# Kernel optimization log

Hardware: AMD Instinct MI355X
Metric: run time of the kernel (lower is better)

The kernel has to match this reference:

```python
import jax, jax.numpy as jnp
from jax import lax
import numpy as np

STYLE_STRENGTH = 1.0
PATCH = 3
TOL = 1e-14


def covsqrt_mean(feature, inverse=False):
    # feature: [b, c, h, w]; matches torch covsqrt_mean with eigenvalue truncation.
    b, c, h, w = feature.shape
    f = feature.reshape(b, c, h * w)
    mean = jnp.mean(f, axis=2, keepdims=True)
    zm = f - mean
    cov = jnp.einsum('bcn,bdn->bcd', zm, zm)  # unnormalized covariance, [b,c,c]
    evals, evecs = jnp.linalg.eigh(cov)       # ascending evals, like torch
    p = -0.5 if inverse else 0.5
    # torch keeps evals[k:] where k is the first index with eval > tol; since
    # evals are sorted ascending this equals masking evals > tol.
    mask = evals > TOL
    d = jnp.where(mask, jnp.where(mask, evals, 1.0) ** p, 0.0)
    covsqrt = jnp.einsum('bij,bj,bkj->bik', evecs, d, evecs)
    return covsqrt, mean


def whitening(feature):
    b, c, h, w = feature.shape
    inv_cs, mean = covsqrt_mean(feature, inverse=True)
    out = jnp.einsum('bcd,bdn->bcn', inv_cs, feature.reshape(b, c, -1) - mean)
    return out.reshape(b, c, h, w)


def coloring(feature, target):
    b, c, h, w = feature.shape
    cs, mean = covsqrt_mean(target, inverse=False)
    out = jnp.einsum('bcd,bdn->bcn', cs, feature.reshape(b, c, -1)) + mean
    return out.reshape(b, c, h, w)


def extract_kernels(feat, k):
    # feat [b,c,h,w] -> per-location style patches as conv kernels [b, h*w, c, k, k]
    b, c, h, w = feat.shape
    pad = (k - 1) // 2
    fp = jnp.pad(feat, ((0, 0), (0, 0), (pad, pad), (pad, pad)))
    # stack the k*k shifted views: [b, c, h, w, k*k] in (ky, kx) row-major order,
    # matching torch unfold(2,k).unfold(3,k) flattening.
    patches = jnp.stack([fp[:, :, dy:dy + h, dx:dx + w]
                         for dy in range(k) for dx in range(k)], axis=-1)
    return patches.reshape(b, c, h * w, k * k).transpose(0, 2, 1, 3).reshape(b, h * w, c, k, k)


def reassemble(norm_c, norm_s, k):
    b, c, h, w = norm_c.shape
    ker = extract_kernels(norm_s, k)                                  # [b, hw_s, c, k, k]
    knorm = jnp.sqrt(jnp.sum(ker ** 2, axis=(2, 3, 4), keepdims=True))
    pad = (k - 1) // 2

    def conv_one(feat, kk):
        # feat [c,h,w], kk [hw_s,c,k,k] -> score [hw_s,h,w]
        x = jnp.pad(feat, ((0, 0), (pad, pad), (pad, pad)))[None]
        return lax.conv_general_dilated(x, kk, (1, 1), 'VALID')[0]

    score = jax.vmap(conv_one)(norm_c, ker / knorm)                   # [b, hw_s, h, w]
    idx = jnp.argmax(score, axis=1)                                   # [b, h, w]
    onehot = jax.nn.one_hot(idx, score.shape[1], dtype=score.dtype).transpose(0, 3, 1, 2)

    def deconv_one(oh, kk):
        # conv_transpose2d(padded onehot, kk, padding=k-1) == VALID conv with
        # spatially flipped kernel (in/out channels swapped).
        x = jnp.pad(oh, ((0, 0), (pad, pad), (pad, pad)))[None]        # [1, hw_s, h+2p, w+2p]
        wf = jnp.flip(kk, axis=(2, 3)).transpose(1, 0, 2, 3)           # [c, hw_s, k, k]
        return lax.conv_general_dilated(x, wf, (1, 1), 'VALID')[0]     # [c, h, w]

    out = jax.vmap(deconv_one)(onehot, ker)                           # [b, c, h, w]
    # overlap-count normalization: separable box filter of ones
    cnt_h = jnp.convolve(jnp.ones(h, out.dtype), jnp.ones(k, out.dtype), mode='same')
    cnt_w = jnp.convolve(jnp.ones(w, out.dtype), jnp.ones(k, out.dtype), mode='same')
    deconv_norm = (cnt_h[:, None] * cnt_w[None, :])[None, None]
    return out / deconv_norm


def setup_inputs() -> dict:
    key = jax.random.key(0)
    k1, k2 = jax.random.split(key)
    b, ch, h, w = 2, 256, 48, 48
    c = jax.random.normal(k1, (b, ch, h, w), dtype=jnp.float32)
    s = jax.random.normal(k2, (b, ch, h, w), dtype=jnp.float32)
    return {'c': c, 's': s}


def reference(c, s):
    norm_c = whitening(c)
    norm_s = whitening(s)
    rF = reassemble(norm_c, norm_s, PATCH)
    sF = coloring(rF, s)
    return (1.0 - STYLE_STRENGTH) * c + STYLE_STRENGTH * sF
```

## Files before the change

### kernel.cpp

```cpp
#include <hip/hip_runtime.h>
#include <math.h>

#define HW 2304
#define NC 256
#define NPIX 2500
#define NPIXP 2560
#define MATSZ 65536
#define NS_ITERS 5
#define NSLAB 6
#define KSLAB 384
#define PMSZ (2560 * 256)
#define GSZ ((u64)NPIXP * NPIXP)

typedef unsigned long long u64;
typedef unsigned short ushortt;
typedef __attribute__((ext_vector_type(8))) short bhalf8;
typedef __attribute__((ext_vector_type(4))) float f32x4;

__global__ void mean_kernel(const float* __restrict__ c, const float* __restrict__ s,
                            double* __restrict__ mean, double* __restrict__ snorm) {
  int ch = blockIdx.x, m = blockIdx.y;
  const float* src = (m < 2 ? c + m * (NC * HW) : s + (m - 2) * (NC * HW)) + ch * HW;
  double acc = 0.0, acc2 = 0.0;
  for (int n = threadIdx.x; n < HW; n += 64) {
    double v = (double)src[n];
    acc += v; acc2 += v * v;
  }
  for (int o = 32; o > 0; o >>= 1) {
    acc += __shfl_down(acc, o);
    acc2 += __shfl_down(acc2, o);
  }
  if (threadIdx.x == 0) {
    mean[m * NC + ch] = acc / (double)HW;
    double diag = acc2 - acc * acc / (double)HW;
    atomicAdd(&snorm[m], 1.25 * diag / 256.0);
  }
}

__launch_bounds__(256)
__global__ void cov_part(const float* __restrict__ c, const float* __restrict__ s,
                         float* __restrict__ covp) {
  int z = blockIdx.z;
  int m = z / NSLAB, slab = z % NSLAB;
  const float* src = (m < 2 ? c + m * (NC * HW) : s + (m - 2) * (NC * HW));
  int i0 = blockIdx.y * 64, j0 = blockIdx.x * 64;
  int kb = slab * KSLAB;
  __shared__ float As[16][64], Bs[16][64];
  int tx = threadIdx.x, ty = threadIdx.y;
  int tid = ty * 16 + tx;
  int li = tid >> 2;
  int lk4 = tid & 3;
  float acc[4][4] = {};
  for (int kc = 0; kc < KSLAB; kc += 16) {
    __syncthreads();
    float4 va = *(const float4*)&src[(u64)(i0 + li) * HW + kb + kc + lk4 * 4];
    float4 vb = *(const float4*)&src[(u64)(j0 + li) * HW + kb + kc + lk4 * 4];
    As[lk4 * 4 + 0][li] = va.x; As[lk4 * 4 + 1][li] = va.y;
    As[lk4 * 4 + 2][li] = va.z; As[lk4 * 4 + 3][li] = va.w;
    Bs[lk4 * 4 + 0][li] = vb.x; Bs[lk4 * 4 + 1][li] = vb.y;
    Bs[lk4 * 4 + 2][li] = vb.z; Bs[lk4 * 4 + 3][li] = vb.w;
    __syncthreads();
    #pragma unroll
    for (int kk = 0; kk < 16; ++kk) {
      float4 a = *(const float4*)&As[kk][ty * 4];
      float4 b = *(const float4*)&Bs[kk][tx * 4];
      float av[4] = {a.x, a.y, a.z, a.w};
      float bv[4] = {b.x, b.y, b.z, b.w};
      #pragma unroll
      for (int i = 0; i < 4; ++i)
        #pragma unroll
        for (int j = 0; j < 4; ++j) acc[i][j] += av[i] * bv[j];
    }
  }
  float* Cp = covp + (u64)z * MATSZ;
  #pragma unroll
  for (int i = 0; i < 4; ++i) {
    float4 v = make_float4(acc[i][0], acc[i][1], acc[i][2], acc[i][3]);
    *(float4*)&Cp[(i0 + ty * 4 + i) * NC + j0 + tx * 4] = v;
  }
}

__global__ void cov_reduce(const float* __restrict__ covp, const double* __restrict__ mean,
                           const double* __restrict__ snorm,
                           float* __restrict__ Y0, float* __restrict__ Z1) {
  int m = blockIdx.y;
  int row = blockIdx.x, col = threadIdx.x;
  int e = row * 256 + col;
  float v = 0.0f;
  #pragma unroll
  for (int slab = 0; slab < NSLAB; ++slab)
    v += covp[(u64)(m * NSLAB + slab) * MATSZ + e];
  double mi = mean[m * NC + row], mj = mean[m * NC + col];
  float res = (float)((double)v - (double)HW * mi * mj);
  float inv = (float)(1.0 / snorm[m]);
  float y0 = res * inv;
  Y0[m * MATSZ + e] = y0;
  Z1[m * MATSZ + e] = ((row == col) ? 1.5f : 0.0f) - 0.5f * y0;
}

__launch_bounds__(256)
__global__ void ns_gemm_Y(const float* __restrict__ Y0, const float* __restrict__ T0,
                          float* __restrict__ Y1) {
  int m = blockIdx.z;
  const float* A = Y0 + m * MATSZ;
  const float* B = T0 + m * MATSZ;
  float* Cp = Y1 + m * MATSZ;
  int m0 = blockIdx.y * 32, n0 = blockIdx.x * 32;
  __shared__ float As[32][33], Bs[32][33];
  int tx = threadIdx.x, ty = threadIdx.y;
  int tid = ty * 16 + tx;
  float acc[2][2] = {};
  for (int k0 = 0; k0 < 256; k0 += 32) {
    __syncthreads();
    #pragma unroll
    for (int l = 0; l < 4; ++l) {
      int idx = tid + l * 256;
      int r = idx >> 5, cc = idx & 31;
      As[r][cc] = A[(m0 + r) * NC + k0 + cc];
      Bs[r][cc] = B[(k0 + r) * NC + n0 + cc];
    }
    __syncthreads();
    #pragma unroll
    for (int kk = 0; kk < 32; ++kk) {
      float a0 = As[ty][kk], a1 = As[ty + 16][kk];
      float b0 = Bs[kk][tx], b1 = Bs[kk][tx + 16];
      acc[0][0] += a0 * b0; acc[0][1] += a0 * b1;
      acc[1][0] += a1 * b0; acc[1][1] += a1 * b1;
    }
  }
  #pragma unroll
  for (int i = 0; i < 2; ++i)
    #pragma unroll
    for (int j = 0; j < 2; ++j)
      Cp[(m0 + ty + 16 * i) * NC + n0 + tx + 16 * j] = acc[i][j];
}

__launch_bounds__(256)
__global__ void ns_gemm_T(const float* __restrict__ Zc, const float* __restrict__ Yc,
                          float* __restrict__ T) {
  int m = blockIdx.z;
  const float* A = Zc + m * MATSZ;
  const float* B = Yc + m * MATSZ;
  int m0 = blockIdx.y * 32, n0 = blockIdx.x * 32;
  __shared__ float As[32][33], Bs[32][33];
  int tx = threadIdx.x, ty = threadIdx.y;
  int tid = ty * 16 + tx;
  float acc[2][2] = {};
  for (int k0 = 0; k0 < 256; k0 += 32) {
    __syncthreads();
    #pragma unroll
    for (int l = 0; l < 4; ++l) {
      int idx = tid + l * 256;
      int r = idx >> 5, cc = idx & 31;
      As[r][cc] = A[(m0 + r) * NC + k0 + cc];
      Bs[r][cc] = B[(k0 + r) * NC + n0 + cc];
    }
    __syncthreads();
    #pragma unroll
    for (int kk = 0; kk < 32; ++kk) {
      float a0 = As[ty][kk], a1 = As[ty + 16][kk];
      float b0 = Bs[kk][tx], b1 = Bs[kk][tx + 16];
      acc[0][0] += a0 * b0; acc[0][1] += a0 * b1;
      acc[1][0] += a1 * b0; acc[1][1] += a1 * b1;
    }
  }
  float* Cp = T + m * MATSZ;
  #pragma unroll
  for (int i = 0; i < 2; ++i)
    #pragma unroll
    for (int j = 0; j < 2; ++j) {
      int row = m0 + ty + 16 * i, col = n0 + tx + 16 * j;
      Cp[row * NC + col] = (row == col ? 1.5f : 0.0f) - 0.5f * acc[i][j];
    }
}

__launch_bounds__(256)
__global__ void ns_gemm_YZ(const float* __restrict__ Yc, const float* __restrict__ Zc,
                           const float* __restrict__ T,
                           float* __restrict__ Yn, float* __restrict__ Zn) {
  int z = blockIdx.z;
  int m = z & 3;
  bool isY = (z < 4);
  const float* A = isY ? (Yc + m * MATSZ) : (T + m * MATSZ);
  const float* B = isY ? (T + m * MATSZ) : (Zc + m * MATSZ);
  float* Cp = isY ? (Yn + m * MATSZ) : (Zn + m * MATSZ);
  int m0 = blockIdx.y * 32, n0 = blockIdx.x * 32;
  __shared__ float As[32][33], Bs[32][33];
  int tx = threadIdx.x, ty = threadIdx.y;
  int tid = ty * 16 + tx;
  float acc[2][2] = {};
  for (int k0 = 0; k0 < 256; k0 += 32) {
    __syncthreads();
    #pragma unroll
    for (int l = 0; l < 4; ++l) {
      int idx = tid + l * 256;
      int r = idx >> 5, cc = idx & 31;
      As[r][cc] = A[(m0 + r) * NC + k0 + cc];
      Bs[r][cc] = B[(k0 + r) * NC + n0 + cc];
    }
    __syncthreads();
    #pragma unroll
    for (int kk = 0; kk < 32; ++kk) {
      float a0 = As[ty][kk], a1 = As[ty + 16][kk];
      float b0 = Bs[kk][tx], b1 = Bs[kk][tx + 16];
      acc[0][0] += a0 * b0; acc[0][1] += a0 * b1;
      acc[1][0] += a1 * b0; acc[1][1] += a1 * b1;
    }
  }
  #pragma unroll
  for (int i = 0; i < 2; ++i)
    #pragma unroll
    for (int j = 0; j < 2; ++j)
      Cp[(m0 + ty + 16 * i) * NC + n0 + tx + 16 * j] = acc[i][j];
}

__launch_bounds__(256)
__global__ void whiten_kernel(const float* __restrict__ c, const float* __restrict__ s,
                              const float* __restrict__ Zf,
                              const double* __restrict__ snorm, const double* __restrict__ mean,
                              float* __restrict__ padC_cf, float* __restrict__ padS_cf,
                              float* __restrict__ padS_cl) {
  int mat = blockIdx.z;
  const float* src = (mat < 2 ? c + mat * (NC * HW) : s + (mat - 2) * (NC * HW));
  const float* A = Zf + mat * MATSZ;
  const double* mn = mean + mat * NC;
  float wscale = (float)(1.0 / sqrt(snorm[mat]));
  int m0 = blockIdx.y * 64, n0 = blockIdx.x * 64;
  __shared__ float As[16][68], Bs[16][68];
  int tid = threadIdx.x;
  int tx = tid & 15, ty = tid >> 4;
  int li = tid >> 2, lk4 = tid & 3;
  int kr = tid >> 4, p4 = (tid & 15) * 4;
  float acc[4][4] = {};
  for (int kc = 0; kc < 256; kc += 16) {
    __syncthreads();
    float4 va = *(const float4*)&A[(u64)(m0 + li) * NC + kc + lk4 * 4];
    As[lk4 * 4 + 0][li] = va.x; As[lk4 * 4 + 1][li] = va.y;
    As[lk4 * 4 + 2][li] = va.z; As[lk4 * 4 + 3][li] = va.w;
    float mk = (float)mn[kc + kr];
    float4 vb = *(const float4*)&src[(u64)(kc + kr) * HW + n0 + p4];
    vb.x -= mk; vb.y -= mk; vb.z -= mk; vb.w -= mk;
    *(float4*)&Bs[kr][p4] = vb;
    __syncthreads();
    #pragma unroll
    for (int kk = 0; kk < 16; ++kk) {
      float4 a = *(const float4*)&As[kk][ty * 4];
      float4 b = *(const float4*)&Bs[kk][tx * 4];
      float av[4] = {a.x, a.y, a.z, a.w};
      float bv[4] = {b.x, b.y, b.z, b.w};
      #pragma unroll
      for (int i = 0; i < 4; ++i)
        #pragma unroll
        for (int j = 0; j < 4; ++j) acc[i][j] += av[i] * bv[j];
    }
  }
  #pragma unroll
  for (int i = 0; i < 4; ++i) {
    int row = m0 + ty * 4 + i;
    #pragma unroll
    for (int j = 0; j < 4; ++j) {
      int n = n0 + tx * 4 + j;
      float v = acc[i][j] * wscale;
      int y = n / 48, x = n % 48;
      int ppos = (y + 1) * 50 + (x + 1);
      if (mat < 2) {
        padC_cf[(u64)mat * (NC * NPIXP) + row * NPIXP + ppos] = v;
      } else {
        padS_cf[(u64)(mat - 2) * (NC * NPIXP) + row * NPIXP + ppos] = v;
        padS_cl[(u64)(mat - 2) * (NPIX * NC) + ppos * NC + row] = v;
      }
    }
  }
}

__launch_bounds__(256)
__global__ void tsplit_kernel(const float* __restrict__ padC_cf, const float* __restrict__ padS_cf,
                              ushortt* __restrict__ padCk_hi, ushortt* __restrict__ padCk_lo,
                              ushortt* __restrict__ padSk_hi, ushortt* __restrict__ padSk_lo,
                              float* __restrict__ ssq) {
  int p0 = blockIdx.x * 64;
  int by = blockIdx.y;
  const float* src = (by < 2) ? padC_cf + (u64)by * (NC * NPIXP)
                              : padS_cf + (u64)(by - 2) * (NC * NPIXP);
  ushortt* dhi = (by < 2) ? padCk_hi + (u64)by * PMSZ : padSk_hi + (u64)(by - 2) * PMSZ;
  ushortt* dlo = (by < 2) ? padCk_lo + (u64)by * PMSZ : padSk_lo + (u64)(by - 2) * PMSZ;
  __shared__ float Tk[64][68];
  int tid = threadIdx.x;
  int rr = tid >> 4, c4 = (tid & 15) * 4;
  int p = tid >> 2, kg = (tid & 3) * 16;
  float sq = 0.0f;
  for (int ks = 0; ks < 256; ks += 64) {
    __syncthreads();
    #pragma unroll
    for (int it = 0; it < 4; ++it) {
      int r = rr + it * 16;
      *(float4*)&Tk[r][c4] = *(const float4*)&src[(u64)(ks + r) * NPIXP + p0 + c4];
    }
    __syncthreads();
    __align__(16) ushortt h[16], lo[16];
    #pragma unroll
    for (int e = 0; e < 16; ++e) {
      float v = Tk[kg + e][p];
      sq += v * v;
      unsigned bb = __float_as_uint(v);
      unsigned hu = (bb + 0x7FFFu + ((bb >> 16) & 1u)) >> 16;
      float hf = __uint_as_float(hu << 16);
      float rres = v - hf;
      unsigned lb = __float_as_uint(rres);
      unsigned lu = (lb + 0x7FFFu + ((lb >> 16) & 1u)) >> 16;
      h[e] = (ushortt)hu;
      lo[e] = (ushortt)lu;
    }
    u64 off = (u64)(p0 + p) * 256 + ks + kg;
    *(uint4*)&dhi[off] = *(const uint4*)&h[0];
    *(uint4*)&dhi[off + 8] = *(const uint4*)&h[8];
    *(uint4*)&dlo[off] = *(const uint4*)&lo[0];
    *(uint4*)&dlo[off + 8] = *(const uint4*)&lo[8];
  }
  sq += __shfl_down(sq, 2);
  sq += __shfl_down(sq, 1);
  if (by >= 2 && (tid & 3) == 0 && (p0 + p) < NPIX)
    ssq[(u64)(by - 2) * NPIX + p0 + p] = sq;
}

__launch_bounds__(256)
__global__ void gram_mfma(const ushortt* __restrict__ Ah_b, const ushortt* __restrict__ Al_b,
                          const ushortt* __restrict__ Bh_b, const ushortt* __restrict__ Bl_b,
                          float* __restrict__ Gb) {
  int bz = blockIdx.z;
  const ushortt* Ah_g = Ah_b + (u64)bz * PMSZ;
  const ushortt* Al_g = Al_b + (u64)bz * PMSZ;
  const ushortt* Bh_g = Bh_b + (u64)bz * PMSZ;
  const ushortt* Bl_g = Bl_b + (u64)bz * PMSZ;
  float* G = Gb + (u64)bz * GSZ;
  __shared__ ushortt As_hi[128 * 32], As_lo[128 * 32], Bs_hi[64 * 32], Bs_lo[64 * 32];
  int tid = threadIdx.x;
  int wv = tid >> 6, l = tid & 63, lr = l & 15, lk = l >> 4;
  int p0 = blockIdx.x * 128, q0 = blockIdx.y * 64;
  int arow = tid >> 2;
  int apart = (tid & 3) * 8;
  const ushortt* pAh0 = Ah_g + (u64)(p0 + arow) * 256 + apart;
  const ushortt* pAh1 = Ah_g + (u64)(p0 + arow + 64) * 256 + apart;
  const ushortt* pAl0 = Al_g + (u64)(p0 + arow) * 256 + apart;
  const ushortt* pAl1 = Al_g + (u64)(p0 + arow + 64) * 256 + apart;
  const ushortt* pBh  = Bh_g + (u64)(q0 + arow) * 256 + apart;
  const ushortt* pBl  = Bl_g + (u64)(q0 + arow) * 256 + apart;
  float4 rAh0 = *(const float4*)pAh0;
  float4 rAh1 = *(const float4*)pAh1;
  float4 rAl0 = *(const float4*)pAl0;
  float4 rAl1 = *(const float4*)pAl1;
  float4 rBh  = *(const float4*)pBh;
  float4 rBl  = *(const float4*)pBl;
  f32x4 acc[2][4];
  #pragma unroll
  for (int a = 0; a < 2; ++a)
    #pragma unroll
    for (int b = 0; b < 4; ++b)
      #pragma unroll
      for (int e = 0; e < 4; ++e) acc[a][b][e] = 0.0f;
  for (int k0 = 0; k0 < 256; k0 += 32) {
    __syncthreads();
    *(float4*)&As_hi[arow * 32 + apart] = rAh0;
    *(float4*)&As_hi[(arow + 64) * 32 + apart] = rAh1;
    *(float4*)&As_lo[arow * 32 + apart] = rAl0;
    *(float4*)&As_lo[(arow + 64) * 32 + apart] = rAl1;
    *(float4*)&Bs_hi[arow * 32 + apart] = rBh;
    *(float4*)&Bs_lo[arow * 32 + apart] = rBl;
    __syncthreads();
    if (k0 + 32 < 256) {
      rAh0 = *(const float4*)(pAh0 + k0 + 32);
      rAh1 = *(const float4*)(pAh1 + k0 + 32);
      rAl0 = *(const float4*)(pAl0 + k0 + 32);
      rAl1 = *(const float4*)(pAl1 + k0 + 32);
      rBh  = *(const float4*)(pBh + k0 + 32);
      rBl  = *(const float4*)(pBl + k0 + 32);
    }
    bhalf8 Ah[2], Al[2], Bh[4], Bl[4];
    #pragma unroll
    for (int a = 0; a < 2; ++a) {
      int off = (wv * 32 + a * 16 + lr) * 32 + lk * 8;
      Ah[a] = *(const bhalf8*)&As_hi[off];
      Al[a] = *(const bhalf8*)&As_lo[off];
    }
    #pragma unroll
    for (int b = 0; b < 4; ++b) {
      int off = (b * 16 + lr) * 32 + lk * 8;
      Bh[b] = *(const bhalf8*)&Bs_hi[off];
      Bl[b] = *(const bhalf8*)&Bs_lo[off];
    }
    #pragma unroll
    for (int a = 0; a < 2; ++a)
      #pragma unroll
      for (int b = 0; b < 4; ++b) {
        acc[a][b] = __builtin_amdgcn_mfma_f32_16x16x32_bf16(Ah[a], Bh[b], acc[a][b], 0, 0, 0);
        acc[a][b] = __builtin_amdgcn_mfma_f32_16x16x32_bf16(Ah[a], Bl[b], acc[a][b], 0, 0, 0);
        acc[a][b] = __builtin_amdgcn_mfma_f32_16x16x32_bf16(Al[a], Bh[b], acc[a][b], 0, 0, 0);
      }
  }
  #pragma unroll
  for (int a = 0; a < 2; ++a)
    #pragma unroll
    for (int b = 0; b < 4; ++b)
      #pragma unroll
      for (int r = 0; r < 4; ++r) {
        int p = p0 + wv * 32 + a * 16 + lk * 4 + r;
        int q = q0 + b * 16 + lr;
        G[(u64)p * NPIXP + q] = acc[a][b][r];
      }
}

__launch_bounds__(256)
__global__ void scoremax_kernel(const float* __restrict__ Gb, const float* __restrict__ ssq,
                                u64* __restrict__ rmax) {
  int y = blockIdx.x, ys = blockIdx.y, b = blockIdx.z;
  const float* G = Gb + (u64)b * GSZ;
  const float* sq = ssq + (u64)b * NPIX;
  __shared__ float Gt[3][50][50];
  __shared__ float sc[48][48];
  __shared__ float sr[152];
  __shared__ float rkl[48];
  int tid = threadIdx.x;
  for (int t = tid; t < 7500; t += 256) {
    int dy = t / 2500, rem = t % 2500;
    int u = rem / 50, v = rem - u * 50;
    Gt[dy][u][v] = G[(u64)((y + dy) * 50 + u) * NPIXP + (ys + dy) * 50 + v];
  }
  if (tid < 150) {
    int dy = tid / 50, v = tid - dy * 50;
    sr[dy * 50 + v] = sq[(ys + dy) * 50 + v];
  }
  __syncthreads();
  if (tid < 48) {
    float t = 0.0f;
    #pragma unroll
    for (int dy = 0; dy < 3; ++dy)
      #pragma unroll
      for (int dx = 0; dx < 3; ++dx) t += sr[dy * 50 + tid + dx];
    rkl[tid] = 1.0f / sqrtf(t);
  }
  __syncthreads();
  #pragma unroll
  for (int k = 0; k < 9; ++k) {
    int idx = tid + k * 256;
    int x = idx / 48, xs = idx - x * 48;
    float v = 0.0f;
    #pragma unroll
    for (int dy = 0; dy < 3; ++dy)
      #pragma unroll
      for (int dx = 0; dx < 3; ++dx)
        v += Gt[dy][x + dx][xs + dx];
    sc[x][xs] = v * rkl[xs];
  }
  __syncthreads();
  if (tid < 48) {
    float best = -1e30f; int bxs = 0;
    for (int xs = 0; xs < 48; ++xs) {
      float v = sc[tid][xs];
      if (v > best) { best = v; bxs = xs; }
    }
    int ps = ys * 48 + bxs;
    unsigned ub = __float_as_uint(best);
    unsigned enc = (ub & 0x80000000u) ? ~ub : (ub | 0x80000000u);
    u64 key = ((u64)enc << 32) | (u64)(2303 - ps);
    atomicMax(&rmax[(u64)b * HW + y * 48 + tid], key);
  }
}

__global__ void reassemble_kernel(const float* __restrict__ padS_cl, const u64* __restrict__ rmax,
                                  float* __restrict__ rF_cl) {
  int pix = blockIdx.x, b = blockIdx.y;
  int y = pix / 48, x = pix % 48;
  const u64* rm = rmax + (u64)b * HW;
  const float* S = padS_cl + (u64)b * (NPIX * NC);
  int ch = threadIdx.x;
  float sum = 0.0f;
  #pragma unroll
  for (int i = 0; i < 3; ++i)
    #pragma unroll
    for (int j = 0; j < 3; ++j) {
      int yn = y + 1 - i, xn = x + 1 - j;
      if (yn >= 0 && yn < 48 && xn >= 0 && xn < 48) {
        int ps = 2303 - (int)(unsigned)(rm[yn * 48 + xn] & 0xFFFFFFFFu);
        int ys = ps / 48, xs = ps % 48;
        sum += S[((ys + i) * 50 + xs + j) * NC + ch];
      }
    }
  float cy = (y == 0 || y == 47) ? 2.0f : 3.0f;
  float cx = (x == 0 || x == 47) ? 2.0f : 3.0f;
  rF_cl[(u64)b * (HW * NC) + pix * NC + ch] = sum / (cy * cx);
}

__launch_bounds__(256)
__global__ void coloring_kernel(const float* __restrict__ Yf, const double* __restrict__ snorm,
                                const double* __restrict__ mean, const float* __restrict__ rF_cl,
                                float* __restrict__ out) {
  int b = blockIdx.z;
  const float* A = Yf + (2 + b) * MATSZ;
  const float* Bp = rF_cl + (u64)b * (HW * NC);
  const double* mn = mean + (2 + b) * NC;
  float cscale = (float)sqrt(snorm[2 + b]);
  int m0 = blockIdx.y * 64, n0 = blockIdx.x * 64;
  __shared__ float As[16][68], Bs[16][68];
  int tid = threadIdx.x;
  int tx = tid & 15, ty = tid >> 4;
  int li = tid >> 2, lk4 = tid & 3;
  int pix = tid >> 2, kq = (tid & 3) * 4;
  float acc[4][4] = {};
  for (int kc = 0; kc < 256; kc += 16) {
    __syncthreads();
    float4 va = *(const float4*)&A[(u64)(m0 + li) * NC + kc + lk4 * 4];
    As[lk4 * 4 + 0][li] = va.x; As[lk4 * 4 + 1][li] = va.y;
    As[lk4 * 4 + 2][li] = va.z; As[lk4 * 4 + 3][li] = va.w;
    float4 vb = *(const float4*)&Bp[(u64)(n0 + pix) * NC + kc + kq];
    Bs[kq + 0][pix] = vb.x; Bs[kq + 1][pix] = vb.y;
    Bs[kq + 2][pix] = vb.z; Bs[kq + 3][pix] = vb.w;
    __syncthreads();
    #pragma unroll
    for (int kk = 0; kk < 16; ++kk) {
      float4 a = *(const float4*)&As[kk][ty * 4];
      float4 b2 = *(const float4*)&Bs[kk][tx * 4];
      float av[4] = {a.x, a.y, a.z, a.w};
      float bv[4] = {b2.x, b2.y, b2.z, b2.w};
      #pragma unroll
      for (int i = 0; i < 4; ++i)
        #pragma unroll
        for (int j = 0; j < 4; ++j) acc[i][j] += av[i] * bv[j];
    }
  }
  #pragma unroll
  for (int i = 0; i < 4; ++i) {
    int row = m0 + ty * 4 + i;
    float madd = (float)mn[row];
    float4 v = make_float4(acc[i][0] * cscale + madd, acc[i][1] * cscale + madd,
                           acc[i][2] * cscale + madd, acc[i][3] * cscale + madd);
    *(float4*)&out[(u64)b * (NC * HW) + (u64)row * HW + n0 + tx * 4] = v;
  }
}

extern "C" void kernel_launch(void* const* d_in, const int* in_sizes, int n_in,
                              void* d_out, int out_size, void* d_ws, size_t ws_size,
                              hipStream_t stream) {
  const float* c = (const float*)d_in[0];
  const float* s = (const float*)d_in[1];
  float* out = (float*)d_out;

  char* ws = (char*)d_ws;
  size_t off = 0;
  auto alloc = [&](size_t bytes) {
    void* p = ws + off;
    off = (off + bytes + 255) & ~(size_t)255;
    return p;
  };
  double* mean   = (double*)alloc(4 * NC * sizeof(double));
  float* covp    = (float*)alloc((size_t)4 * NSLAB * MATSZ * sizeof(float));
  float* Ya      = (float*)alloc((size_t)4 * MATSZ * sizeof(float));
  float* Yb      = (float*)alloc((size_t)4 * MATSZ * sizeof(float));
  float* Za      = (float*)alloc((size_t)4 * MATSZ * sizeof(float));
  float* Zb      = (float*)alloc((size_t)4 * MATSZ * sizeof(float));
  float* T       = (float*)alloc((size_t)4 * MATSZ * sizeof(float));
  float* padC_cf = (float*)alloc((size_t)2 * NC * NPIXP * sizeof(float));
  float* padS_cf = (float*)alloc((size_t)2 * NC * NPIXP * sizeof(float));
  float* padS_cl = (float*)alloc((size_t)2 * NPIX * NC * sizeof(float));
  ushortt* padCk_hi = (ushortt*)alloc((size_t)2 * PMSZ * sizeof(ushortt));
  ushortt* padCk_lo = (ushortt*)alloc((size_t)2 * PMSZ * sizeof(ushortt));
  ushortt* padSk_hi = (ushortt*)alloc((size_t)2 * PMSZ * sizeof(ushortt));
  ushortt* padSk_lo = (ushortt*)alloc((size_t)2 * PMSZ * sizeof(ushortt));
  float* ssq     = (float*)alloc((size_t)2 * NPIX * sizeof(float));
  float* rF_cl   = (float*)alloc((size_t)2 * HW * NC * sizeof(float));
  float* G       = (float*)alloc((size_t)2 * GSZ * sizeof(float));
  u64*   rmax    = (u64*)alloc((size_t)2 * HW * sizeof(u64));
  double* snorm  = (double*)alloc(4 * sizeof(double));

  size_t padBytes = (size_t)(2 * NC * NPIXP + 2 * NC * NPIXP + 2 * NPIX * NC) * sizeof(float);
  hipMemsetAsync(padC_cf, 0, padBytes, stream);
  hipMemsetAsync(rmax, 0, (size_t)2 * HW * sizeof(u64) + 4 * sizeof(double), stream);

  mean_kernel<<<dim3(256, 4), 64, 0, stream>>>(c, s, mean, snorm);
  cov_part<<<dim3(4, 4, 4 * NSLAB), dim3(16, 16), 0, stream>>>(c, s, covp);
  cov_reduce<<<dim3(256, 4), 256, 0, stream>>>(covp, mean, snorm, Ya, Za);
  ns_gemm_Y<<<dim3(8, 8, 4), dim3(16, 16), 0, stream>>>(Ya, Za, Yb);

  float *Yc = Yb, *Zc = Za, *Yn = Ya, *Zn = Zb;
  for (int it = 1; it < NS_ITERS; ++it) {
    ns_gemm_T<<<dim3(8, 8, 4), dim3(16, 16), 0, stream>>>(Zc, Yc, T);
    ns_gemm_YZ<<<dim3(8, 8, 8), dim3(16, 16), 0, stream>>>(Yc, Zc, T, Yn, Zn);
    float* t1 = Yc; Yc = Yn; Yn = t1;
    float* t2 = Zc; Zc = Zn; Zn = t2;
  }

  whiten_kernel<<<dim3(36, 4, 4), 256, 0, stream>>>(c, s, Zc, snorm, mean,
                                                    padC_cf, padS_cf, padS_cl);
  tsplit_kernel<<<dim3(40, 4), 256, 0, stream>>>(padC_cf, padS_cf,
                                                 padCk_hi, padCk_lo, padSk_hi, padSk_lo, ssq);

  gram_mfma<<<dim3(20, 40, 2), 256, 0, stream>>>(padCk_hi, padCk_lo, padSk_hi, padSk_lo, G);
  scoremax_kernel<<<dim3(48, 48, 2), 256, 0, stream>>>(G, ssq, rmax);

  reassemble_kernel<<<dim3(2304, 2), 256, 0, stream>>>(padS_cl, rmax, rF_cl);
  coloring_kernel<<<dim3(36, 4, 2), 256, 0, stream>>>(Yc, snorm, mean, rF_cl, out);
}
```

Measured before the change: 322.1 us.

## Tile scoremax along Gram diagonals to reuse loaded blocks across rows

The score-max kernel now assigns each block a diagonal offset and a run of up to four consecutive output rows. It loads 6 Gram 50x50 blocks into shared memory and reuses them for all four rows, instead of loading 3 blocks per single row. This cuts global reads of the Gram matrix by about half. The argmax across 48 candidate columns is also split over 4 threads per row with shuffle reduction. In exchange, shared memory use per block rises to about 70KB, which may lower occupancy, and many blocks on short diagonals exit early.

```diff
diff --git a/kernel.cpp b/kernel.cpp
--- a/kernel.cpp
+++ b/kernel.cpp
@@ -412,57 +412,79 @@
 __launch_bounds__(256)
 __global__ void scoremax_kernel(const float* __restrict__ Gb, const float* __restrict__ ssq,
                                 u64* __restrict__ rmax) {
-  int y = blockIdx.x, ys = blockIdx.y, b = blockIdx.z;
+  int j = blockIdx.x, cidx = blockIdx.y, b = blockIdx.z;
+  int c = cidx - 47;
+  int y_lo = c < 0 ? -c : 0;
+  int y_hi = c < 0 ? 47 : 47 - c;
+  int yt0 = y_lo + j * 4;
+  if (yt0 > y_hi) return;
+  int ny = min(4, y_hi - yt0 + 1);
+  int nb = ny + 2;
   const float* G = Gb + (u64)b * GSZ;
   const float* sq = ssq + (u64)b * NPIX;
-  __shared__ float Gt[3][50][50];
-  __shared__ float sc[48][48];
-  __shared__ float sr[152];
+  __shared__ float bands[6][2500];
+  __shared__ float ssqb[6][52];
+  __shared__ float sc[48][52];
   __shared__ float rkl[48];
   int tid = threadIdx.x;
-  for (int t = tid; t < 7500; t += 256) {
-    int dy = t / 2500, rem = t % 2500;
+  for (int e = tid; e < nb * 2500; e += 256) {
+    int bi = e / 2500, rem = e - bi * 2500;
     int u = rem / 50, v = rem - u * 50;
-    Gt[dy][u][v] = G[(u64)((y + dy) * 50 + u) * NPIXP + (ys + dy) * 50 + v];
-  }
-  if (tid < 150) {
-    int dy = tid / 50, v = tid - dy * 50;
-    sr[dy * 50 + v] = sq[(ys + dy) * 50 + v];
+    int a = yt0 + bi;
+    bands[bi][rem] = G[(u64)(a * 50 + u) * NPIXP + (a + c) * 50 + v];
+  }
+  for (int e = tid; e < nb * 50; e += 256) {
+    int bi = e / 50, v = e - bi * 50;
+    ssqb[bi][v] = sq[(yt0 + bi + c) * 50 + v];
   }
   __syncthreads();
-  if (tid < 48) {
-    float t = 0.0f;
-    #pragma unroll
-    for (int dy = 0; dy < 3; ++dy)
-      #pragma unroll
-      for (int dx = 0; dx < 3; ++dx) t += sr[dy * 50 + tid + dx];
-    rkl[tid] = 1.0f / sqrtf(t);
-  }
-  __syncthreads();
-  #pragma unroll
-  for (int k = 0; k < 9; ++k) {
-    int idx = tid + k * 256;
-    int x = idx / 48, xs = idx - x * 48;
-    float v = 0.0f;
-    #pragma unroll
-    for (int dy = 0; dy < 3; ++dy)
-      #pragma unroll
-      for (int dx = 0; dx < 3; ++dx)
-        v += Gt[dy][x + dx][xs + dx];
-    sc[x][xs] = v * rkl[xs];
-  }
-  __syncthreads();
-  if (tid < 48) {
-    float best = -1e30f; int bxs = 0;
-    for (int xs = 0; xs < 48; ++xs) {
-      float v = sc[tid][xs];
-      if (v > best) { best = v; bxs = xs; }
-    }
-    int ps = ys * 48 + bxs;
-    unsigned ub = __float_as_uint(best);
-    unsigned enc = (ub & 0x80000000u) ? ~ub : (ub | 0x80000000u);
-    u64 key = ((u64)enc << 32) | (u64)(2303 - ps);
-    atomicMax(&rmax[(u64)b * HW + y * 48 + tid], key);
+  for (int jj = 0; jj < ny; ++jj) {
+    int y = yt0 + jj, ys = y + c;
+    #pragma unroll
+    for (int k = 0; k < 9; ++k) {
+      int idx = tid + k * 256;
+      int x = idx / 48, xs = idx - x * 48;
+      float v = 0.0f;
+      #pragma unroll
+      for (int dy = 0; dy < 3; ++dy)
+        #pragma unroll
+        for (int dx = 0; dx < 3; ++dx)
+          v += bands[jj + dy][(x + dx) * 50 + xs + dx];
+      sc[x][xs] = v;
+    }
+    if (tid < 48) {
+      float t = 0.0f;
+      #pragma unroll
+      for (int dy = 0; dy < 3; ++dy)
+        #pragma unroll
+        for (int dx = 0; dx < 3; ++dx) t += ssqb[jj + dy][tid + dx];
+      rkl[tid] = 1.0f / sqrtf(t);
+    }
+    __syncthreads();
+    if (tid < 192) {
+      int r = tid >> 2, part = tid & 3;
+      float best = -1e30f; int bxs = 0;
+      #pragma unroll
+      for (int i = 0; i < 12; ++i) {
+        int xs = part * 12 + i;
+        float v = sc[r][xs] * rkl[xs];
+        if (v > best) { best = v; bxs = xs; }
+      }
+      #pragma unroll
+      for (int o = 1; o < 4; o <<= 1) {
+        float ov = __shfl_down(best, o);
+        int oi = __shfl_down(bxs, o);
+        if (ov > best || (ov == best && oi < bxs)) { best = ov; bxs = oi; }
+      }
+      if (part == 0) {
+        int ps = ys * 48 + bxs;
+        unsigned ub = __float_as_uint(best);
+        unsigned enc = (ub & 0x80000000u) ? ~ub : (ub | 0x80000000u);
+        u64 key = ((u64)enc << 32) | (u64)(2303 - ps);
+        atomicMax(&rmax[(u64)b * HW + y * 48 + r], key);
+      }
+    }
+    __syncthreads();
   }
 }
 
@@ -594,7 +616,7 @@
                                                  padCk_hi, padCk_lo, padSk_hi, padSk_lo, ssq);
 
   gram_mfma<<<dim3(20, 40, 2), 256, 0, stream>>>(padCk_hi, padCk_lo, padSk_hi, padSk_lo, G);
-  scoremax_kernel<<<dim3(48, 48, 2), 256, 0, stream>>>(G, ssq, rmax);
+  scoremax_kernel<<<dim3(12, 95, 2), 256, 0, stream>>>(G, ssq, rmax);
 
   reassemble_kernel<<<dim3(2304, 2), 256, 0, stream>>>(padS_cl, rmax, rF_cl);
   coloring_kernel<<<dim3(36, 4, 2), 256, 0, stream>>>(Yc, snorm, mean, rF_cl, out);
```

Result: slower. 334.3 us (+3.8%).
